# Optimization experiments

Hardware: AMD Instinct MI355X
Metric: run time of the kernel (lower is better)

The kernel has to match this reference:

```python
import jax, jax.numpy as jnp
import numpy as np

IN_DIM = 256
QK_DIM = IN_DIM // 8


def setup_inputs() -> dict:
    key = jax.random.key(0)
    ks = jax.random.split(key, 6)
    x = jax.random.normal(ks[0], (8, IN_DIM, 64, 64), dtype=jnp.float32)
    # 1x1 conv == per-pixel linear; store weights as [out, in]
    q_w = jax.random.normal(ks[1], (QK_DIM, IN_DIM), dtype=jnp.float32) * (1.0 / np.sqrt(IN_DIM))
    q_b = jax.random.normal(ks[2], (QK_DIM,), dtype=jnp.float32) * 0.01
    v_w = jax.random.normal(ks[3], (IN_DIM, IN_DIM), dtype=jnp.float32) * (1.0 / np.sqrt(IN_DIM))
    v_b = jax.random.normal(ks[4], (IN_DIM,), dtype=jnp.float32) * 0.01
    gamma = jnp.zeros((1,), dtype=jnp.float32) + 0.5  # nonzero so attention branch contributes
    return {"x": x, "q_w": q_w, "q_b": q_b, "v_w": v_w, "v_b": v_b, "gamma": gamma}


def reference(x, q_w, q_b, v_w, v_b, gamma):
    b, c, h, w = x.shape
    n = h * w
    xf = x.reshape(b, c, n)                                    # [b, c, n]
    # NOTE: original forward uses q_conv for BOTH q and k (k_conv unused)
    q = jnp.einsum('oc,bcn->bon', q_w, xf) + q_b[None, :, None]  # [b, d, n]
    proj_q = jnp.transpose(q, (0, 2, 1))                       # [b, n, d]
    energy = jnp.einsum('bid,bdj->bij', proj_q, q)             # [b, n, n]
    attention = jax.nn.softmax(energy, axis=-1)
    v = jnp.einsum('oc,bcn->bon', v_w, xf) + v_b[None, :, None]  # [b, c, n]
    # out[b,c,i] = sum_j v[b,c,j] * attention[b,i,j]
    out = jnp.einsum('bcj,bij->bci', v, attention)
    out = out.reshape(b, c, h, w)
    return gamma * out + x
```

## Files before the change

kernel.cpp:

```cpp
#include <hip/hip_runtime.h>

#define B_   8
#define C_   256
#define D_   32
#define N_   4096
#define FMX  64.0f

typedef __attribute__((ext_vector_type(8))) short bf8_t;
typedef __attribute__((ext_vector_type(4))) float f4_t;

__device__ __forceinline__ unsigned short f2bf(float f) {
    unsigned int u = __builtin_bit_cast(unsigned int, f);
    u += 0x7FFFu + ((u >> 16) & 1u);
    return (unsigned short)(u >> 16);
}
__device__ __forceinline__ float bf2f(unsigned short h) {
    unsigned int u = ((unsigned int)h) << 16;
    return __builtin_bit_cast(float, u);
}
__device__ __forceinline__ uint4 pack8(const unsigned short* h) {
    uint4 u;
    u.x = h[0] | ((unsigned)h[1] << 16); u.y = h[2] | ((unsigned)h[3] << 16);
    u.z = h[4] | ((unsigned)h[5] << 16); u.w = h[6] | ((unsigned)h[7] << 16);
    return u;
}

__global__ __launch_bounds__(256) void wprep_kernel(
    const float* __restrict__ qw, const float* __restrict__ vw,
    unsigned short* __restrict__ wqFh, unsigned short* __restrict__ wqFl,
    unsigned short* __restrict__ wvF)
{
    const int tid = blockIdx.x * 256 + threadIdx.x;
    if (tid < 8192) {
        const int k = tid;
        const int rowblk = k >> 9, kk = (k >> 6) & 7, lane = k & 63;
        const int oc = rowblk * 16 + (lane & 15), c0 = kk * 32 + (lane >> 4) * 8;
        const float* src = vw + oc * 256 + c0;
        unsigned short h[8];
        #pragma unroll
        for (int e = 0; e < 8; ++e) h[e] = f2bf(src[e]);
        *(uint4*)(wvF + (size_t)k * 8) = pack8(h);
    } else if (tid < 9216) {
        const int k = tid - 8192;
        const int rowblk = k >> 9, kk = (k >> 6) & 7, lane = k & 63;
        const int oc = rowblk * 16 + (lane & 15), c0 = kk * 32 + (lane >> 4) * 8;
        const float* src = qw + oc * 256 + c0;
        unsigned short h[8], l[8];
        #pragma unroll
        for (int e = 0; e < 8; ++e) {
            h[e] = f2bf(src[e]);
            l[e] = f2bf(src[e] - bf2f(h[e]));
        }
        *(uint4*)(wqFh + (size_t)k * 8) = pack8(h);
        *(uint4*)(wqFl + (size_t)k * 8) = pack8(l);
    }
}

__global__ __launch_bounds__(256, 2) void proj_kernel(
    const float* __restrict__ x, const unsigned short* __restrict__ wqFh,
    const unsigned short* __restrict__ wqFl, const unsigned short* __restrict__ wvF,
    const float* __restrict__ qb, const float* __restrict__ vb,
    unsigned short* __restrict__ qh, unsigned short* __restrict__ ql,
    unsigned short* __restrict__ vT)
{
    __shared__ __align__(16) unsigned short S[18432];

    const int t    = threadIdx.x;
    const int lane = t & 63;
    const int w    = t >> 6;
    const int q4   = lane >> 4;
    const int l15  = lane & 15;
    const int b    = blockIdx.x >> 6;
    const int tile = blockIdx.x & 63;
    const int i0   = tile * 64;

    const float* xb = x + (size_t)b * C_ * N_ + i0 + lane;
    #pragma unroll
    for (int cc = 0; cc < 8; ++cc) {
        const int chi = w * 8 + cc;
        float v[8];
        #pragma unroll
        for (int e = 0; e < 8; ++e) v[e] = xb[(size_t)(chi * 8 + e) * N_];
        unsigned short h[8];
        #pragma unroll
        for (int e = 0; e < 8; ++e) h[e] = f2bf(v[e]);
        *(uint4*)&S[(chi * 64 + lane) * 8] = pack8(h);
    }
    __syncthreads();

    f4_t acc[4][4];
    #pragma unroll
    for (int mt = 0; mt < 4; ++mt)
        #pragma unroll
        for (int nt = 0; nt < 4; ++nt) acc[mt][nt] = (f4_t)0.0f;
    f4_t qacc[2];
    qacc[0] = (f4_t)0.0f; qacc[1] = (f4_t)0.0f;

    #pragma unroll
    for (int kk = 0; kk < 8; ++kk) {
        bf8_t Bh[4];
        #pragma unroll
        for (int nt = 0; nt < 4; ++nt)
            Bh[nt] = *(const bf8_t*)&S[((kk * 4 + q4) * 64 + nt * 16 + l15) * 8];
        bf8_t Av[4];
        #pragma unroll
        for (int mt = 0; mt < 4; ++mt)
            Av[mt] = *(const bf8_t*)&wvF[(size_t)(((w * 4 + mt) * 8 + kk) * 64 + lane) * 8];
        bf8_t Aqh[2], Aql[2];
        #pragma unroll
        for (int mq = 0; mq < 2; ++mq) {
            Aqh[mq] = *(const bf8_t*)&wqFh[(size_t)((mq * 8 + kk) * 64 + lane) * 8];
            Aql[mq] = *(const bf8_t*)&wqFl[(size_t)((mq * 8 + kk) * 64 + lane) * 8];
        }

        #pragma unroll
        for (int mt = 0; mt < 4; ++mt)
            #pragma unroll
            for (int nt = 0; nt < 4; ++nt)
                acc[mt][nt] = __builtin_amdgcn_mfma_f32_16x16x32_bf16(
                    Av[mt], Bh[nt], acc[mt][nt], 0, 0, 0);
        #pragma unroll
        for (int mq = 0; mq < 2; ++mq) {
            qacc[mq] = __builtin_amdgcn_mfma_f32_16x16x32_bf16(Aqh[mq], Bh[w], qacc[mq], 0, 0, 0);
            qacc[mq] = __builtin_amdgcn_mfma_f32_16x16x32_bf16(Aql[mq], Bh[w], qacc[mq], 0, 0, 0);
        }
    }

    {
        const int iq = i0 + w * 16 + l15;
        #pragma unroll
        for (int mq = 0; mq < 2; ++mq) {
            float4 qb4 = *(const float4*)(qb + mq * 16 + q4 * 4);
            float qv[4] = {qacc[mq][0] + qb4.x, qacc[mq][1] + qb4.y,
                           qacc[mq][2] + qb4.z, qacc[mq][3] + qb4.w};
            unsigned short hr[4], lr[4];
            #pragma unroll
            for (int r = 0; r < 4; ++r) {
                hr[r] = f2bf(qv[r]);
                lr[r] = f2bf(qv[r] - bf2f(hr[r]));
            }
            uint2 uh, ul;
            uh.x = hr[0] | ((unsigned)hr[1] << 16); uh.y = hr[2] | ((unsigned)hr[3] << 16);
            ul.x = lr[0] | ((unsigned)lr[1] << 16); ul.y = lr[2] | ((unsigned)lr[3] << 16);
            size_t qoff = ((size_t)b * N_ + iq) * D_ + mq * 16 + q4 * 4;
            *(uint2*)(qh + qoff) = uh;
            *(uint2*)(ql + qoff) = ul;
        }
    }

    __syncthreads();
    #pragma unroll
    for (int mt = 0; mt < 4; ++mt) {
        float4 vb4 = *(const float4*)(vb + w * 64 + mt * 16 + q4 * 4);
        float bias[4] = {vb4.x, vb4.y, vb4.z, vb4.w};
        #pragma unroll
        for (int nt = 0; nt < 4; ++nt)
            #pragma unroll
            for (int r = 0; r < 4; ++r)
                S[(w * 64 + mt * 16 + q4 * 4 + r) * 72 + nt * 16 + l15] =
                    f2bf(acc[mt][nt][r] + bias[r]);
    }
    __syncthreads();
    #pragma unroll
    for (int k2 = 0; k2 < 8; ++k2) {
        int id = k2 * 256 + t;
        int oc = id >> 3, seg = id & 7;
        uint4 dat = *(const uint4*)&S[oc * 72 + seg * 8];
        *(uint4*)(vT + ((size_t)b * C_ + oc) * N_ + i0 + seg * 8) = dat;
    }
}

__global__ __launch_bounds__(256, 2) void attn_kernel(
    const unsigned short* __restrict__ qh, const unsigned short* __restrict__ ql,
    const unsigned short* __restrict__ vT, const float* __restrict__ x,
    const float* __restrict__ gamma_p, float* __restrict__ out)
{
    __shared__ __align__(16) unsigned short Vs[8 * 257 * 8];
    __shared__ __align__(16) unsigned short Pb[8 * 64 * 8];
    __shared__ __align__(16) float rowl[64];

    float* T = (float*)Vs;

    const int t    = threadIdx.x;
    const int lane = t & 63;
    const int w    = t >> 6;
    const int q4   = lane >> 4;
    const int l15  = lane & 15;
    const int b    = blockIdx.x >> 6;
    const int i0   = (blockIdx.x & 63) * 64;

    const unsigned short* qhb = qh + (size_t)b * N_ * D_;
    const unsigned short* qlb = ql + (size_t)b * N_ * D_;
    const unsigned short* vTb = vT + (size_t)b * C_ * N_;

    bf8_t Ah[4], Al[4];
    #pragma unroll
    for (int mt = 0; mt < 4; ++mt) {
        size_t off = (size_t)(i0 + mt * 16 + l15) * D_ + q4 * 8;
        Ah[mt] = *(const bf8_t*)(qhb + off);
        Al[mt] = *(const bf8_t*)(qlb + off);
    }

    f4_t acc[4][4];
    #pragma unroll
    for (int mt = 0; mt < 4; ++mt)
        #pragma unroll
        for (int nt = 0; nt < 4; ++nt) acc[mt][nt] = (f4_t)0.0f;

    f4_t lacc[4];
    #pragma unroll
    for (int mt = 0; mt < 4; ++mt) lacc[mt] = (f4_t)0.0f;
    bf8_t onesb;
    #pragma unroll
    for (int e = 0; e < 8; ++e) onesb[e] = (short)0x3F80;

    for (int jt = 0; jt < N_ / 64; ++jt) {
        const int j0 = jt * 64;

        size_t koff = (size_t)(j0 + w * 16 + l15) * D_ + q4 * 8;
        bf8_t Bh = *(const bf8_t*)(qhb + koff);
        bf8_t Bl = *(const bf8_t*)(qlb + koff);

        __syncthreads();

        #pragma unroll
        for (int r = 0; r < 8; ++r) {
            int idx = r * 256 + t;
            int c = idx >> 3, part = idx & 7;
            uint4 d = *(const uint4*)(vTb + (size_t)c * N_ + j0 + part * 8);
            *(uint4*)(&Vs[(part * 257 + c) * 8]) = d;
        }

        f4_t s[4];
        #pragma unroll
        for (int mt = 0; mt < 4; ++mt) {
            f4_t a = (f4_t)0.0f;
            a = __builtin_amdgcn_mfma_f32_16x16x32_bf16(Ah[mt], Bh, a, 0, 0, 0);
            a = __builtin_amdgcn_mfma_f32_16x16x32_bf16(Ah[mt], Bl, a, 0, 0, 0);
            a = __builtin_amdgcn_mfma_f32_16x16x32_bf16(Al[mt], Bh, a, 0, 0, 0);
            s[mt] = a;
        }

        const int jl = w * 16 + l15;
        const int pprt = jl >> 3, jlo = jl & 7;
        #pragma unroll
        for (int mt = 0; mt < 4; ++mt)
            #pragma unroll
            for (int r = 0; r < 4; ++r) {
                float p = __expf(s[mt][r] - FMX);
                Pb[(pprt * 64 + mt * 16 + q4 * 4 + r) * 8 + jlo] = f2bf(p);
            }

        __syncthreads();

        #pragma unroll
        for (int kk = 0; kk < 2; ++kk) {
            bf8_t Af[4], Bf[4];
            #pragma unroll
            for (int mt = 0; mt < 4; ++mt)
                Af[mt] = *(const bf8_t*)(&Pb[((kk * 4 + q4) * 64 + mt * 16 + l15) * 8]);
            #pragma unroll
            for (int nt = 0; nt < 4; ++nt)
                Bf[nt] = *(const bf8_t*)(&Vs[((kk * 4 + q4) * 257 + w * 64 + nt * 16 + l15) * 8]);
            #pragma unroll
            for (int mt = 0; mt < 4; ++mt)
                #pragma unroll
                for (int nt = 0; nt < 4; ++nt)
                    acc[mt][nt] = __builtin_amdgcn_mfma_f32_16x16x32_bf16(
                        Af[mt], Bf[nt], acc[mt][nt], 0, 0, 0);
            if (w == 3) {
                #pragma unroll
                for (int mt = 0; mt < 4; ++mt)
                    lacc[mt] = __builtin_amdgcn_mfma_f32_16x16x32_bf16(
                        Af[mt], onesb, lacc[mt], 0, 0, 0);
            }
        }
    }

    __syncthreads();
    if (w == 3 && l15 == 0) {
        #pragma unroll
        for (int mt = 0; mt < 4; ++mt)
            #pragma unroll
            for (int r = 0; r < 4; ++r)
                rowl[mt * 16 + q4 * 4 + r] = lacc[mt][r];
    }
    __syncthreads();

    const float g = gamma_p[0];
    for (int mt = 0; mt < 4; ++mt) {
        float4 rl = *(float4*)(&rowl[mt * 16 + q4 * 4]);
        float inv[4] = { g / rl.x, g / rl.y, g / rl.z, g / rl.w };
        #pragma unroll
        for (int nt = 0; nt < 4; ++nt)
            #pragma unroll
            for (int r = 0; r < 4; ++r)
                T[(w * 64 + nt * 16 + l15) * 17 + q4 * 4 + r] = acc[mt][nt][r] * inv[r];
        __syncthreads();
        #pragma unroll
        for (int pass = 0; pass < 4; ++pass) {
            int c  = pass * 64 + (t >> 2);
            int ii = (t & 3) * 4;
            float4 o;
            o.x = T[c * 17 + ii];     o.y = T[c * 17 + ii + 1];
            o.z = T[c * 17 + ii + 2]; o.w = T[c * 17 + ii + 3];
            size_t goff = ((size_t)b * C_ + c) * N_ + i0 + mt * 16 + ii;
            float4 xv = *(const float4*)(x + goff);
            o.x += xv.x; o.y += xv.y; o.z += xv.z; o.w += xv.w;
            *(float4*)(out + goff) = o;
        }
        __syncthreads();
    }
}

extern "C" void kernel_launch(void* const* d_in, const int* in_sizes, int n_in,
                              void* d_out, int out_size, void* d_ws, size_t ws_size,
                              hipStream_t stream)
{
    const float* x     = (const float*)d_in[0];
    const float* q_w   = (const float*)d_in[1];
    const float* q_b   = (const float*)d_in[2];
    const float* v_w   = (const float*)d_in[3];
    const float* v_b   = (const float*)d_in[4];
    const float* gamma = (const float*)d_in[5];
    float* out = (float*)d_out;

    unsigned short* ws16 = (unsigned short*)d_ws;
    unsigned short* qhp  = ws16;
    unsigned short* qlp  = ws16 + 1048576;
    unsigned short* vTp  = ws16 + 2097152;
    unsigned short* wvF  = ws16 + 10485760;
    unsigned short* wqFh = wvF + 65536;
    unsigned short* wqFl = wqFh + 8192;

    wprep_kernel<<<36, 256, 0, stream>>>(q_w, v_w, wqFh, wqFl, wvF);
    proj_kernel<<<B_ * (N_ / 64), 256, 0, stream>>>(x, wqFh, wqFl, wvF, q_b, v_b,
                                                    qhp, qlp, vTp);
    attn_kernel<<<B_ * (N_ / 64), 256, 0, stream>>>(qhp, qlp, vTp, x, gamma, out);
}
```

Before: 233.9 us.

## Double-buffer V and P tiles to use one barrier per key tile

The attention loop now walks 32-key tiles instead of 64, with V and P shared-memory buffers split into two alternating halves. Each iteration issues only one __syncthreads instead of two. The QK^T score work is redistributed so each wave computes two row tiles for one 16-key column slice, which balances exp work across waves. The change halves the per-iteration MFMA depth and doubles the iteration count, and correctness relies on the double buffering to avoid write-after-read races. The trailing barrier before the rowl write was also removed; it looks safe because T aliases Vs[0] and there is still a barrier before T is used.

```diff
diff --git a/kernel.cpp b/kernel.cpp
--- a/kernel.cpp
+++ b/kernel.cpp
@@ -175,11 +175,11 @@
     const unsigned short* __restrict__ vT, const float* __restrict__ x,
     const float* __restrict__ gamma_p, float* __restrict__ out)
 {
-    __shared__ __align__(16) unsigned short Vs[8 * 257 * 8];
-    __shared__ __align__(16) unsigned short Pb[8 * 64 * 8];
+    __shared__ __align__(16) unsigned short Vs[2][4 * 257 * 8];
+    __shared__ __align__(16) unsigned short Pb[2][4 * 64 * 8];
     __shared__ __align__(16) float rowl[64];
 
-    float* T = (float*)Vs;
+    float* T = (float*)&Vs[0][0];
 
     const int t    = threadIdx.x;
     const int lane = t & 63;
@@ -193,12 +193,15 @@
     const unsigned short* qlb = ql + (size_t)b * N_ * D_;
     const unsigned short* vTb = vT + (size_t)b * C_ * N_;
 
-    bf8_t Ah[4], Al[4];
-    #pragma unroll
-    for (int mt = 0; mt < 4; ++mt) {
-        size_t off = (size_t)(i0 + mt * 16 + l15) * D_ + q4 * 8;
-        Ah[mt] = *(const bf8_t*)(qhb + off);
-        Al[mt] = *(const bf8_t*)(qlb + off);
+    const int mh = (w >> 1) << 1;
+    const int nw = w & 1;
+
+    bf8_t Ah[2], Al[2];
+    #pragma unroll
+    for (int m = 0; m < 2; ++m) {
+        size_t off = (size_t)(i0 + (mh + m) * 16 + l15) * D_ + q4 * 8;
+        Ah[m] = *(const bf8_t*)(qhb + off);
+        Al[m] = *(const bf8_t*)(qlb + off);
     }
 
     f4_t acc[4][4];
@@ -214,70 +217,67 @@
     #pragma unroll
     for (int e = 0; e < 8; ++e) onesb[e] = (short)0x3F80;
 
-    for (int jt = 0; jt < N_ / 64; ++jt) {
-        const int j0 = jt * 64;
-
-        size_t koff = (size_t)(j0 + w * 16 + l15) * D_ + q4 * 8;
+    #pragma unroll 2
+    for (int jt = 0; jt < N_ / 32; ++jt) {
+        const int buf = jt & 1;
+        const int j0  = jt * 32;
+
+        size_t koff = (size_t)(j0 + nw * 16 + l15) * D_ + q4 * 8;
         bf8_t Bh = *(const bf8_t*)(qhb + koff);
         bf8_t Bl = *(const bf8_t*)(qlb + koff);
 
+        {
+            const unsigned short* vsrc = vTb + j0 + (t & 3) * 8;
+            #pragma unroll
+            for (int r = 0; r < 4; ++r) {
+                int c = r * 64 + (t >> 2);
+                uint4 d = *(const uint4*)(vsrc + (size_t)c * N_);
+                *(uint4*)&Vs[buf][((t & 3) * 257 + c) * 8] = d;
+            }
+        }
+
+        f4_t s[2];
+        #pragma unroll
+        for (int m = 0; m < 2; ++m) {
+            f4_t a = (f4_t)0.0f;
+            a = __builtin_amdgcn_mfma_f32_16x16x32_bf16(Ah[m], Bh, a, 0, 0, 0);
+            a = __builtin_amdgcn_mfma_f32_16x16x32_bf16(Ah[m], Bl, a, 0, 0, 0);
+            a = __builtin_amdgcn_mfma_f32_16x16x32_bf16(Al[m], Bh, a, 0, 0, 0);
+            s[m] = a;
+        }
+
+        const int part = nw * 2 + (l15 >> 3), jlo = l15 & 7;
+        #pragma unroll
+        for (int m = 0; m < 2; ++m)
+            #pragma unroll
+            for (int r = 0; r < 4; ++r) {
+                float p = __expf(s[m][r] - FMX);
+                Pb[buf][(part * 64 + (mh + m) * 16 + q4 * 4 + r) * 8 + jlo] = f2bf(p);
+            }
+
         __syncthreads();
 
-        #pragma unroll
-        for (int r = 0; r < 8; ++r) {
-            int idx = r * 256 + t;
-            int c = idx >> 3, part = idx & 7;
-            uint4 d = *(const uint4*)(vTb + (size_t)c * N_ + j0 + part * 8);
-            *(uint4*)(&Vs[(part * 257 + c) * 8]) = d;
-        }
-
-        f4_t s[4];
-        #pragma unroll
-        for (int mt = 0; mt < 4; ++mt) {
-            f4_t a = (f4_t)0.0f;
-            a = __builtin_amdgcn_mfma_f32_16x16x32_bf16(Ah[mt], Bh, a, 0, 0, 0);
-            a = __builtin_amdgcn_mfma_f32_16x16x32_bf16(Ah[mt], Bl, a, 0, 0, 0);
-            a = __builtin_amdgcn_mfma_f32_16x16x32_bf16(Al[mt], Bh, a, 0, 0, 0);
-            s[mt] = a;
-        }
-
-        const int jl = w * 16 + l15;
-        const int pprt = jl >> 3, jlo = jl & 7;
-        #pragma unroll
-        for (int mt = 0; mt < 4; ++mt)
-            #pragma unroll
-            for (int r = 0; r < 4; ++r) {
-                float p = __expf(s[mt][r] - FMX);
-                Pb[(pprt * 64 + mt * 16 + q4 * 4 + r) * 8 + jlo] = f2bf(p);
-            }
-
-        __syncthreads();
-
-        #pragma unroll
-        for (int kk = 0; kk < 2; ++kk) {
-            bf8_t Af[4], Bf[4];
+        bf8_t Af[4], Bf[4];
+        #pragma unroll
+        for (int mt = 0; mt < 4; ++mt)
+            Af[mt] = *(const bf8_t*)&Pb[buf][(q4 * 64 + mt * 16 + l15) * 8];
+        #pragma unroll
+        for (int nt = 0; nt < 4; ++nt)
+            Bf[nt] = *(const bf8_t*)&Vs[buf][(q4 * 257 + w * 64 + nt * 16 + l15) * 8];
+        #pragma unroll
+        for (int mt = 0; mt < 4; ++mt)
+            #pragma unroll
+            for (int nt = 0; nt < 4; ++nt)
+                acc[mt][nt] = __builtin_amdgcn_mfma_f32_16x16x32_bf16(
+                    Af[mt], Bf[nt], acc[mt][nt], 0, 0, 0);
+        if (w == 3) {
             #pragma unroll
             for (int mt = 0; mt < 4; ++mt)
-                Af[mt] = *(const bf8_t*)(&Pb[((kk * 4 + q4) * 64 + mt * 16 + l15) * 8]);
-            #pragma unroll
-            for (int nt = 0; nt < 4; ++nt)
-                Bf[nt] = *(const bf8_t*)(&Vs[((kk * 4 + q4) * 257 + w * 64 + nt * 16 + l15) * 8]);
-            #pragma unroll
-            for (int mt = 0; mt < 4; ++mt)
-                #pragma unroll
-                for (int nt = 0; nt < 4; ++nt)
-                    acc[mt][nt] = __builtin_amdgcn_mfma_f32_16x16x32_bf16(
-                        Af[mt], Bf[nt], acc[mt][nt], 0, 0, 0);
-            if (w == 3) {
-                #pragma unroll
-                for (int mt = 0; mt < 4; ++mt)
-                    lacc[mt] = __builtin_amdgcn_mfma_f32_16x16x32_bf16(
-                        Af[mt], onesb, lacc[mt], 0, 0, 0);
-            }
-        }
-    }
-
-    __syncthreads();
+                lacc[mt] = __builtin_amdgcn_mfma_f32_16x16x32_bf16(
+                    Af[mt], onesb, lacc[mt], 0, 0, 0);
+        }
+    }
+
     if (w == 3 && l15 == 0) {
         #pragma unroll
         for (int mt = 0; mt < 4; ++mt)
```

Result: slower. 273.6 us (+17.0%).
